# Kernel optimization log

Measured on AMD Instinct MI355X. Metric: run time of the kernel, lower is better.

## Reference

```python
import jax, jax.numpy as jnp
import numpy as np

C = 1024        # number of classes
N = 8           # proxies per class
ALLNUM = C * N  # 8192 total proxies
DIM = 512
R = 0.05
TOPK = int(np.ceil(R * ALLNUM))  # 410
LAM = 0.3
B = 2048


def setup_inputs() -> dict:
    key = jax.random.key(0)
    k1, k2, k3 = jax.random.split(key, 3)
    inp = jax.random.normal(k1, (B, DIM), dtype=jnp.float32)
    target = jax.random.randint(k2, (B,), 0, C, dtype=jnp.int64)
    # kaiming-uniform-initialized proxies approximated by scaled normal init
    proxies = jax.random.normal(k3, (DIM, ALLNUM), dtype=jnp.float32)
    instance_label = jnp.repeat(jnp.arange(C, dtype=jnp.int64), N)  # [ALLNUM]
    return {"input": inp, "target": target, "Proxies": proxies,
            "instance_label": instance_label}


def reference(input, target, Proxies, instance_label):
    # L2-normalize each proxy column (F.normalize along dim=0, eps=1e-12)
    norm = jnp.maximum(jnp.linalg.norm(Proxies, axis=0, keepdims=True), 1e-12)
    centers = Proxies / norm                             # [DIM, ALLNUM]
    similarity = input @ centers                          # [B, ALLNUM]

    positive_mask = (target[:, None] == instance_label[None, :]).astype(similarity.dtype)
    _, indices = jax.lax.top_k(similarity + 1000.0 * positive_mask, TOPK)  # [B, TOPK]

    rows = jnp.arange(similarity.shape[0])[:, None]
    mask = jnp.zeros_like(similarity).at[rows, indices].set(1.0)
    prob_a = mask * similarity                            # sparse-masked similarities

    y_instance_onehot = jax.nn.one_hot(instance_label, C, dtype=similarity.dtype)  # [ALLNUM, C]
    logits = prob_a @ y_instance_onehot                   # [B, C]

    y_target_onehot = jax.nn.one_hot(target, C, dtype=similarity.dtype)  # [B, C]
    logits_mask = 1.0 - (logits == 0.0).astype(similarity.dtype)

    # scale_mask_softmax with scale=1 along dim=1
    e = jnp.exp(logits) * logits_mask
    predict = e / (1e-8 + jnp.sum(e, axis=1, keepdims=True))
    lossClassify = jnp.mean(jnp.sum(-y_target_onehot * jnp.log(predict + 1e-20), axis=1))

    # proxy regularizer: cross-entropy of proxy-vs-class logits
    simCenter = centers.T @ centers                       # [ALLNUM, ALLNUM]
    centers_logits = simCenter @ y_instance_onehot        # [ALLNUM, C]
    logp = jax.nn.log_softmax(centers_logits, axis=1)
    reg = -jnp.mean(jnp.take_along_axis(logp, instance_label[:, None], axis=1))

    return (lossClassify + LAM * reg, lossClassify)
```

## Files before the change

### kernel.cpp

```cpp
#include <hip/hip_runtime.h>
#include <hip/hip_bf16.h>
#include <math.h>

#define C_CLS   1024
#define NPROXY  8
#define ALLNUM  8192
#define DIM     512
#define TOPK    410
#define LAM     0.3f
#define BATCH   2048

#define BAND_CAP_BLK 28
#define ROW_CAP      512
#define GCAP         64

typedef __bf16 bf16x8 __attribute__((ext_vector_type(8)));
typedef float floatx4 __attribute__((ext_vector_type(4)));
typedef unsigned short ushort_t;

#define WS_RNORM 0
#define WS_SIG   8192
#define WS_LP    10240
#define WS_RP    12288
#define WS_CNT   14336
#define WS_NDEF  16384
#define WS_FLAG  18432
#define WS_CLS   20480
#define WS_BVAL  (WS_CLS + 2048*1024)
#define WS_BCOL  (WS_BVAL + 2048*512)
#define WS_ABF   (WS_BCOL + 2048*256)
#define WS_PBF   (WS_ABF + 524288)
#define WS_STBF  (WS_PBF + 2097152)
#define WS_LOG   (WS_STBF + 262144)

__device__ inline float block_reduce(float v, int is_max, float* red, int t) {
    #pragma unroll
    for (int o = 32; o > 0; o >>= 1) {
        float w = __shfl_down(v, o);
        v = is_max ? fmaxf(v, w) : (v + w);
    }
    __syncthreads();
    if ((t & 63) == 0) red[t >> 6] = v;
    __syncthreads();
    return is_max ? fmaxf(fmaxf(red[0], red[1]), fmaxf(red[2], red[3]))
                  : (red[0] + red[1] + red[2] + red[3]);
}

__device__ inline ushort_t f2bf(float f) {
    unsigned u = __float_as_uint(f);
    return (ushort_t)((u + 0x7FFFu + ((u >> 16) & 1u)) >> 16);
}

__device__ inline float bf2f(ushort_t u) {
    return __uint_as_float(((unsigned)u) << 16);
}

__device__ inline void ld_g2l_16(const void* g, void* l) {
    __builtin_amdgcn_global_load_lds(
        (const __attribute__((address_space(1))) unsigned int*)g,
        (__attribute__((address_space(3))) unsigned int*)l,
        16, 0, 0);
}

__device__ inline unsigned f2ord(float f) {
    unsigned u = __float_as_uint(f);
    return (u & 0x80000000u) ? ~u : (u | 0x80000000u);
}

__global__ __launch_bounds__(256) void k_prep1(const float* __restrict__ P,
                                               const float* __restrict__ input,
                                               float* __restrict__ rnorm,
                                               float* __restrict__ rowsig,
                                               ushort_t* __restrict__ Abf,
                                               ushort_t* __restrict__ Pbf,
                                               unsigned* __restrict__ zaux) {
    __shared__ float tile[32][33];
    float* cred = &tile[0][0];
    int bx = blockIdx.x, t = threadIdx.x;
    if (bx < 256) {
        int tc = t & 31, g = t >> 5;
        int c = bx * 32 + tc;
        const float* pc = P + (size_t)(g * 64) * ALLNUM + c;
        float s = 0.f;
        #pragma unroll 8
        for (int d = 0; d < 64; ++d) {
            float v = pc[(size_t)d * ALLNUM];
            s += v * v;
        }
        cred[g * 32 + tc] = s;
        __syncthreads();
        if (g == 0) {
            float tot = 0.f;
            #pragma unroll
            for (int k = 0; k < 8; ++k) tot += cred[k * 32 + tc];
            rnorm[c] = 1.0f / fmaxf(sqrtf(tot), 1e-12f);
        }
    } else if (bx < 256 + 1024) {
        int a = bx - 256;
        int idx = a * 256 + t;
        float4 v = ((const float4*)input)[idx];
        ushort4 o;
        o.x = f2bf(v.x); o.y = f2bf(v.y); o.z = f2bf(v.z); o.w = f2bf(v.w);
        ((ushort4*)Abf)[idx] = o;
        float sq = v.x * v.x + v.y * v.y + v.z * v.z + v.w * v.w;
        #pragma unroll
        for (int off = 32; off > 0; off >>= 1) sq += __shfl_down(sq, off);
        int lane = t & 63, w = t >> 6;
        if (lane == 0) cred[w] = sq;
        __syncthreads();
        if (t == 0) {
            rowsig[2 * a]     = sqrtf(cred[0] + cred[1]);
            rowsig[2 * a + 1] = sqrtf(cred[2] + cred[3]);
        }
    } else if (bx < 256 + 1024 + 4096) {
        int id = bx - 1280;
        int c0 = (id & 255) * 32, r0 = (id >> 8) * 32;
        int tc = t & 31, tr = t >> 5;
        #pragma unroll
        for (int p = 0; p < 4; ++p)
            tile[tr + p * 8][tc] = P[(size_t)(r0 + tr + p * 8) * ALLNUM + c0 + tc];
        __syncthreads();
        #pragma unroll
        for (int p = 0; p < 4; ++p) {
            int oc = tr + p * 8;
            Pbf[(size_t)(c0 + oc) * DIM + r0 + tc] = f2bf(tile[tc][oc]);
        }
    } else {
        for (int i = t; i < 3 * 2048; i += 256) zaux[i] = 0u;
    }
}

__global__ __launch_bounds__(256) void k_stage2(const ushort_t* __restrict__ A,
                                                const ushort_t* __restrict__ B,
                                                const float* __restrict__ P,
                                                const float* __restrict__ rnorm,
                                                const float* __restrict__ rowsig,
                                                const int* __restrict__ target,
                                                float* __restrict__ g_cls,
                                                float* __restrict__ g_bval,
                                                ushort_t* __restrict__ g_bcol,
                                                unsigned* __restrict__ g_cnt,
                                                unsigned* __restrict__ g_ndef,
                                                unsigned* __restrict__ g_flag,
                                                ushort_t* __restrict__ Stbf) {
    __shared__ __align__(16) ushort_t smem[2 * 128 * 64];
    int bx = blockIdx.x, t = threadIdx.x;

    if (bx < 1024) {
        ushort_t* sA = smem;
        ushort_t* sB = smem + 128 * 64;
        int w = t >> 6, lane = t & 63;
        int wm = w >> 1, wn = w & 1;
        int bj = (bx & 63) * 128, bi = (bx >> 6) * 128;

        floatx4 acc[4][4];
        #pragma unroll
        for (int tm = 0; tm < 4; ++tm)
            #pragma unroll
            for (int tn = 0; tn < 4; ++tn)
                acc[tm][tn] = (floatx4){0.f, 0.f, 0.f, 0.f};

        for (int k0 = 0; k0 < DIM; k0 += 64) {
            #pragma unroll
            for (int it = 0; it < 4; ++it) {
                int c = w * 256 + it * 64 + lane;
                int m = c >> 3, s = c & 7;
                int q = s ^ (m & 7);
                ld_g2l_16(A + ((size_t)(bi + m) << 9) + k0 + q * 8,
                          &sA[(w * 256 + it * 64) * 8]);
            }
            #pragma unroll
            for (int it = 0; it < 4; ++it) {
                int c = w * 256 + it * 64 + lane;
                int m = c >> 3, s = c & 7;
                int q = s ^ (m & 7);
                ld_g2l_16(B + ((size_t)(bj + m) << 9) + k0 + q * 8,
                          &sB[(w * 256 + it * 64) * 8]);
            }
            asm volatile("s_waitcnt vmcnt(0)" ::: "memory");
            __syncthreads();

            #pragma unroll
            for (int kk = 0; kk < 2; ++kk) {
                bf16x8 af[4], bfr[4];
                int ml = lane & 15, q = lane >> 4;
                #pragma unroll
                for (int tm = 0; tm < 4; ++tm) {
                    int m = wm * 64 + tm * 16 + ml;
                    int s = (kk * 4 + q) ^ (m & 7);
                    af[tm] = *(const bf16x8*)&sA[m * 64 + s * 8];
                }
                #pragma unroll
                for (int tn = 0; tn < 4; ++tn) {
                    int n = wn * 64 + tn * 16 + ml;
                    int s = (kk * 4 + q) ^ (n & 7);
                    bfr[tn] = *(const bf16x8*)&sB[n * 64 + s * 8];
                }
                #pragma unroll
                for (int tm = 0; tm < 4; ++tm)
                    #pragma unroll
                    for (int tn = 0; tn < 4; ++tn)
                        acc[tm][tn] = __builtin_amdgcn_mfma_f32_16x16x32_bf16(
                            af[tm], bfr[tn], acc[tm][tn], 0, 0, 0);
            }
            __syncthreads();
        }

        unsigned char* sb = (unsigned char*)smem;
        float*    e_cls = (float*)sb;
        float*    e_bv  = (float*)(sb + 8192);
        ushort_t* e_bc  = (ushort_t*)(sb + 22528);
        unsigned* e_cnt = (unsigned*)(sb + 29696);
        unsigned* e_nd  = (unsigned*)(sb + 30208);

        #pragma unroll
        for (int i = t; i < 2048; i += 256) e_cls[i] = 0.f;
        if (t < 128) { e_cnt[t] = 0u; e_nd[t] = 0u; }
        __syncthreads();

        int ml = lane & 15, qd = lane >> 4;
        #pragma unroll
        for (int tm = 0; tm < 4; ++tm) {
            int rl0 = wm * 64 + tm * 16 + qd * 4;
            int rowb = bi + rl0;
            float4 rs4 = *(const float4*)&rowsig[rowb];
            int4   tg4 = *(const int4*)&target[rowb];
            #pragma unroll
            for (int tn = 0; tn < 4; ++tn) {
                int cl = wn * 64 + tn * 16 + ml;
                int col = bj + cl;
                float sc = rnorm[col];
                int cls = col >> 3;
                int clsl = cl >> 3;
                #pragma unroll
                for (int i = 0; i < 4; ++i) {
                    int rl = rl0 + i;
                    float v = acc[tm][tn][i] * sc;
                    float sg = ((const float*)&rs4)[i] * (1.0f / 22.616f);
                    float hiT = 1.80f * sg, loT = 1.47f * sg;
                    int tg = ((const int*)&tg4)[i];
                    if (cls == tg) {
                        atomicAdd(&e_cls[rl * 16 + clsl], v);
                    } else if (v >= hiT) {
                        atomicAdd(&e_cls[rl * 16 + clsl], v);
                        atomicAdd(&e_nd[rl], 1u);
                    } else if (v >= loT) {
                        unsigned u = atomicAdd(&e_cnt[rl], 1u);
                        if (u < BAND_CAP_BLK) {
                            e_bv[rl * BAND_CAP_BLK + u] = v;
                            e_bc[rl * BAND_CAP_BLK + u] = (ushort_t)col;
                        }
                    }
                }
            }
        }
        __syncthreads();

        int bjc = bj >> 3;
        #pragma unroll
        for (int i = t; i < 2048; i += 256) {
            int rl = i >> 4, c = i & 15;
            g_cls[(size_t)(bi + rl) * C_CLS + bjc + c] = e_cls[i];
        }
        if (t < 128) {
            int row = bi + t;
            unsigned c = e_cnt[t];
            unsigned nd = e_nd[t];
            if (nd) atomicAdd(&g_ndef[row], nd);
            if (c) {
                unsigned cc = (c > BAND_CAP_BLK) ? BAND_CAP_BLK : c;
                unsigned base = atomicAdd(&g_cnt[row], cc);
                if (c > BAND_CAP_BLK || base + cc > ROW_CAP) g_flag[row] = 1u;
                for (unsigned j = 0; j < cc; ++j) {
                    if (base + j >= ROW_CAP) break;
                    g_bval[(size_t)row * ROW_CAP + base + j] = e_bv[t * BAND_CAP_BLK + j];
                    g_bcol[(size_t)row * ROW_CAP + base + j] = e_bc[t * BAND_CAP_BLK + j];
                }
            }
        }
    } else {
        float* tile = (float*)smem;
        int id = bx - 1024;
        int c0 = (id & 31) * 32, d0 = (id >> 5) * 32;
        int cl = t & 31, dl8 = t >> 5;
        #pragma unroll
        for (int p = 0; p < 4; ++p) {
            int d = d0 + dl8 + 8 * p;
            int c = c0 + cl;
            const float* pp = P + (size_t)d * ALLNUM + c * NPROXY;
            const float* rn = rnorm + c * NPROXY;
            float4 a = *(const float4*)pp;
            float4 b = *(const float4*)(pp + 4);
            float4 ra = *(const float4*)rn;
            float4 rb = *(const float4*)(rn + 4);
            tile[(dl8 + 8 * p) * 33 + cl] =
                a.x * ra.x + a.y * ra.y + a.z * ra.z + a.w * ra.w +
                b.x * rb.x + b.y * rb.y + b.z * rb.z + b.w * rb.w;
        }
        __syncthreads();
        #pragma unroll
        for (int p = 0; p < 4; ++p) {
            int cl2 = dl8 + 8 * p, dl2 = t & 31;
            Stbf[(size_t)(c0 + cl2) * DIM + d0 + dl2] = f2bf(tile[dl2 * 33 + cl2]);
        }
    }
}

__device__ inline void suffix_select1(unsigned* s_hist, unsigned kk,
                                      unsigned* s_wtot, unsigned* sh_bin,
                                      unsigned* sh_k, int t, int lane, int wid) {
    unsigned h = s_hist[t];
    unsigned v = h;
    #pragma unroll
    for (int off = 1; off < 64; off <<= 1) {
        unsigned o = __shfl_down(v, off);
        if (lane + off < 64) v += o;
    }
    if (lane == 0) s_wtot[wid] = v;
    __syncthreads();
    unsigned above = v - h;
    for (int w2 = wid + 1; w2 < 4; ++w2) above += s_wtot[w2];
    unsigned cum = above + h;
    if (cum >= kk && above < kk) { *sh_bin = (unsigned)t; *sh_k = kk - above; }
    __syncthreads();
}

__global__ __launch_bounds__(256) void k_stage3(const int* __restrict__ target,
                                                const float* __restrict__ rowsig,
                                                const float* __restrict__ rnorm,
                                                const ushort_t* __restrict__ Abf,
                                                const ushort_t* __restrict__ Pbf,
                                                const ushort_t* __restrict__ Stbf,
                                                const float* __restrict__ g_cls,
                                                const float* __restrict__ g_bval,
                                                const ushort_t* __restrict__ g_bcol,
                                                const unsigned* __restrict__ g_cnt,
                                                const unsigned* __restrict__ g_ndef,
                                                const unsigned* __restrict__ g_flag,
                                                float* __restrict__ loss_part,
                                                ushort_t* __restrict__ logits) {
    __shared__ __align__(16) unsigned char smem[16384];
    int bx = blockIdx.x, t = threadIdx.x;
    int lane = t & 63, wid = t >> 6;

    if (bx < 2048) {
        ushort_t* sA = (ushort_t*)smem;
        ushort_t* sB = (ushort_t*)(smem + 8192);
        int id = bx;
        int bj = (id & 15) * 64;
        int bi = (id >> 4) * 64;
        int w = wid;
        int wm = w >> 1, wn = w & 1;

        floatx4 acc[2][2];
        #pragma unroll
        for (int tm = 0; tm < 2; ++tm)
            #pragma unroll
            for (int tn = 0; tn < 2; ++tn)
                acc[tm][tn] = (floatx4){0.f, 0.f, 0.f, 0.f};

        for (int k0 = 0; k0 < DIM; k0 += 64) {
            #pragma unroll
            for (int it = 0; it < 2; ++it) {
                int c = (w * 2 + it) * 64 + lane;
                int m = c >> 3, s = c & 7;
                int q = s ^ (m & 7);
                ld_g2l_16(Pbf + ((size_t)(bi + m) << 9) + k0 + q * 8,
                          &sA[((w * 2 + it) * 64) * 8]);
            }
            #pragma unroll
            for (int it = 0; it < 2; ++it) {
                int c = (w * 2 + it) * 64 + lane;
                int m = c >> 3, s = c & 7;
                int q = s ^ (m & 7);
                ld_g2l_16(Stbf + ((size_t)(bj + m) << 9) + k0 + q * 8,
                          &sB[((w * 2 + it) * 64) * 8]);
            }
            asm volatile("s_waitcnt vmcnt(0)" ::: "memory");
            __syncthreads();

            #pragma unroll
            for (int kk = 0; kk < 2; ++kk) {
                bf16x8 af[2], bfr[2];
                int ml = lane & 15, q = lane >> 4;
                #pragma unroll
                for (int tm = 0; tm < 2; ++tm) {
                    int m = wm * 32 + tm * 16 + ml;
                    int s = (kk * 4 + q) ^ (m & 7);
                    af[tm] = *(const bf16x8*)&sA[m * 64 + s * 8];
                }
                #pragma unroll
                for (int tn = 0; tn < 2; ++tn) {
                    int n = wn * 32 + tn * 16 + ml;
                    int s = (kk * 4 + q) ^ (n & 7);
                    bfr[tn] = *(const bf16x8*)&sB[n * 64 + s * 8];
                }
                #pragma unroll
                for (int tm = 0; tm < 2; ++tm)
                    #pragma unroll
                    for (int tn = 0; tn < 2; ++tn)
                        acc[tm][tn] = __builtin_amdgcn_mfma_f32_16x16x32_bf16(
                            af[tm], bfr[tn], acc[tm][tn], 0, 0, 0);
            }
            __syncthreads();
        }

        int ml = lane & 15, qd = lane >> 4;
        #pragma unroll
        for (int tm = 0; tm < 2; ++tm) {
            int rowb = bi + wm * 32 + tm * 16 + qd * 4;
            float4 rnr = *(const float4*)&rnorm[rowb];
            #pragma unroll
            for (int tn = 0; tn < 2; ++tn) {
                int col = bj + wn * 32 + tn * 16 + ml;
                #pragma unroll
                for (int i = 0; i < 4; ++i)
                    logits[(size_t)(rowb + i) * C_CLS + col] =
                        f2bf(acc[tm][tn][i] * ((const float*)&rnr)[i]);
            }
        }
    } else {
        float*    s_cls  = (float*)smem;
        float*    s_bval = (float*)(smem + 4096);
        ushort_t* s_bcol = (ushort_t*)(smem + 6144);
        unsigned* s_hist = (unsigned*)(smem + 7168);
        float*    s_arow = (float*)(smem + 8192);
        unsigned* s_wtot = (unsigned*)(smem + 10240);
        unsigned* shv    = (unsigned*)(smem + 10256);
        float*    shf    = (float*)(smem + 10272);
        float*    red    = (float*)(smem + 10288);
        float*    s_gval = (float*)(smem + 10304);

        int b = bx - 2048;
        int tgt = target[b];
        float sig = rowsig[b] * (1.0f / 22.616f);
        float hiT = 1.80f * sig, loT = 1.47f * sig;
        float binscale = 256.0f / (hiT - loT);

        ((float4*)s_cls)[t] = ((const float4*)(g_cls + (size_t)b * C_CLS))[t];
        unsigned cnt = g_cnt[b], nd = g_ndef[b], fl = g_flag[b];
        int kq = (TOPK - NPROXY) - (int)nd;
        int ok = (fl == 0u) && (cnt <= ROW_CAP) && (kq >= 0) && ((int)cnt >= kq);
        if (t == 0) shv[1] = 0u;
        s_hist[t] = 0u;
        __syncthreads();

        if (ok) {
            if (kq > 0) {
                for (int j = t; j < (int)cnt; j += 256) {
                    float v = g_bval[(size_t)b * ROW_CAP + j];
                    s_bval[j] = v;
                    s_bcol[j] = g_bcol[(size_t)b * ROW_CAP + j];
                    int bin = (int)((v - loT) * binscale);
                    bin = (bin > 255) ? 255 : bin;
                    atomicAdd(&s_hist[bin], 1u);
                }
                __syncthreads();
                suffix_select1(s_hist, (unsigned)kq, s_wtot, &shv[2], &shv[3], t, lane, wid);
                int Bb = (int)shv[2];
                int knew = (int)shv[3];
                for (int j = t; j < (int)cnt; j += 256) {
                    float v = s_bval[j];
                    int bin = (int)((v - loT) * binscale);
                    bin = (bin > 255) ? 255 : bin;
                    if (bin == Bb) {
                        unsigned g = atomicAdd(&shv[1], 1u);
                        if (g < GCAP) s_gval[g] = v;
                    }
                }
                __syncthreads();
                int gc = (int)shv[1];
                if (gc <= GCAP) {
                    if (t < gc) {
                        float vj = s_gval[t];
                        unsigned g = 0, geq = 0;
                        for (int i = 0; i < gc; ++i) {
                            float vi = s_gval[i];
                            g   += (vi > vj) ? 1u : 0u;
                            geq += (vi >= vj) ? 1u : 0u;
                        }
                        if (g < (unsigned)knew && geq >= (unsigned)knew) shf[0] = vj;
                    }
                } else {
                    for (int j = t; j < (int)cnt; j += 256) {
                        float vj = s_bval[j];
                        unsigned g = 0, geq = 0;
                        for (int i = 0; i < (int)cnt; ++i) {
                            float vi = s_bval[i];
                            g   += (vi > vj) ? 1u : 0u;
                            geq += (vi >= vj) ? 1u : 0u;
                        }
                        if (g < (unsigned)kq && geq >= (unsigned)kq) shf[0] = vj;
                    }
                }
                __syncthreads();
                float thr = shf[0];
                for (int j = t; j < (int)cnt; j += 256)
                    if (s_bval[j] >= thr)
                        atomicAdd(&s_cls[s_bcol[j] >> 3], s_bval[j]);
            }
        } else {
            for (int i = t; i < DIM; i += 256)
                s_arow[i] = bf2f(Abf[(size_t)b * DIM + i]);
            #pragma unroll
            for (int i = 0; i < 4; ++i) s_cls[t + 256 * i] = 0.f;
            __syncthreads();
            float4 v4[8];
            for (int p = 0; p < 8; ++p) {
                int f = t + 256 * p;
                float vv[4];
                for (int e = 0; e < 4; ++e) {
                    int col = 4 * f + e;
                    const ushort_t* pc = Pbf + (size_t)col * DIM;
                    float a = 0.f;
                    for (int d = 0; d < DIM; ++d)
                        a += s_arow[d] * bf2f(pc[d]);
                    vv[e] = a * rnorm[col];
                }
                float4 o; o.x = vv[0]; o.y = vv[1]; o.z = vv[2]; o.w = vv[3];
                v4[p] = o;
            }
            #pragma unroll
            for (int p = 0; p < 8; ++p) {
                int f = t + 256 * p;
                const float* pv = (const float*)&v4[p];
                if ((f >> 1) == tgt)
                    atomicAdd(&s_cls[tgt], pv[0] + pv[1] + pv[2] + pv[3]);
            }
            unsigned L = 0u, R = 0xFFFFFFFFu;
            for (int it = 0; it < 33 && R - L > 1; ++it) {
                unsigned mid = L + ((R - L) >> 1);
                float c = 0.f;
                #pragma unroll
                for (int p = 0; p < 8; ++p) {
                    int f = t + 256 * p;
                    const float* pv = (const float*)&v4[p];
                    if ((f >> 1) != tgt) {
                        #pragma unroll
                        for (int e = 0; e < 4; ++e)
                            c += (f2ord(pv[e]) >= mid) ? 1.f : 0.f;
                    }
                }
                c = block_reduce(c, 0, red, t);
                if (c >= (float)(TOPK - NPROXY)) L = mid; else R = mid;
                __syncthreads();
            }
            #pragma unroll
            for (int p = 0; p < 8; ++p) {
                int f = t + 256 * p;
                const float* pv = (const float*)&v4[p];
                if ((f >> 1) != tgt) {
                    #pragma unroll
                    for (int e = 0; e < 4; ++e)
                        if (f2ord(pv[e]) >= L)
                            atomicAdd(&s_cls[f >> 1], pv[e]);
                }
            }
        }
        __syncthreads();

        float4 cv = ((const float4*)s_cls)[t];
        float m = -1e30f;
        if (cv.x != 0.0f) m = fmaxf(m, cv.x);
        if (cv.y != 0.0f) m = fmaxf(m, cv.y);
        if (cv.z != 0.0f) m = fmaxf(m, cv.z);
        if (cv.w != 0.0f) m = fmaxf(m, cv.w);
        m = block_reduce(m, 1, red, t);
        float se = 0.f;
        if (cv.x != 0.0f) se += expf(cv.x - m);
        if (cv.y != 0.0f) se += expf(cv.y - m);
        if (cv.z != 0.0f) se += expf(cv.z - m);
        if (cv.w != 0.0f) se += expf(cv.w - m);
        se = block_reduce(se, 0, red, t);
        if (t == 0) {
            float lt = s_cls[tgt];
            float predict_t = expf(lt - m) / (1e-8f * expf(-m) + se);
            loss_part[b] = -logf(predict_t + 1e-20f);
        }
    }
}

__global__ __launch_bounds__(256) void k_regloss(const ushort_t* __restrict__ logits,
                                                 float* __restrict__ reg_part) {
    __shared__ float bsum[4];
    int t = threadIdx.x, lane = t & 63, wid = t >> 6;
    int i = blockIdx.x * 4 + wid;
    const ushort_t* row = logits + (size_t)i * C_CLS;
    uint4 c0 = ((const uint4*)row)[lane];
    uint4 c1 = ((const uint4*)(row + 512))[lane];

    float f[16];
    const unsigned* u0 = (const unsigned*)&c0;
    const unsigned* u1 = (const unsigned*)&c1;
    #pragma unroll
    for (int k = 0; k < 4; ++k) {
        f[2 * k]     = __uint_as_float(u0[k] << 16);
        f[2 * k + 1] = __uint_as_float(u0[k] & 0xFFFF0000u);
        f[8 + 2 * k]     = __uint_as_float(u1[k] << 16);
        f[8 + 2 * k + 1] = __uint_as_float(u1[k] & 0xFFFF0000u);
    }

    int cstar = i >> 3;
    int chunk = cstar >> 9, within = cstar & 511;
    float sd = 0.f;
    if (lane == (within >> 3)) sd = f[chunk * 8 + (within & 7)];

    float m = -1e30f;
    #pragma unroll
    for (int k = 0; k < 16; ++k) m = fmaxf(m, f[k]);
    #pragma unroll
    for (int off = 32; off > 0; off >>= 1) m = fmaxf(m, __shfl_xor(m, off));

    float se = 0.f;
    #pragma unroll
    for (int k = 0; k < 16; ++k) se += expf(f[k] - m);
    #pragma unroll
    for (int off = 32; off > 0; off >>= 1) se += __shfl_xor(se, off);
    #pragma unroll
    for (int off = 32; off > 0; off >>= 1) sd += __shfl_xor(sd, off);

    if (lane == 0) bsum[wid] = m + logf(se) - sd;
    __syncthreads();
    if (t == 0)
        reg_part[blockIdx.x] = bsum[0] + bsum[1] + bsum[2] + bsum[3];
}

__global__ __launch_bounds__(256) void k_final(const float* __restrict__ lp,
                                               const float* __restrict__ rp,
                                               float* __restrict__ out) {
    __shared__ float red[4];
    int t = threadIdx.x;
    float4 a = ((const float4*)lp)[t];
    float4 b = ((const float4*)lp)[t + 256];
    float4 c = ((const float4*)rp)[t];
    float4 d = ((const float4*)rp)[t + 256];
    float ls = a.x + a.y + a.z + a.w + b.x + b.y + b.z + b.w;
    float rs = c.x + c.y + c.z + c.w + d.x + d.y + d.z + d.w;
    ls = block_reduce(ls, 0, red, t);
    rs = block_reduce(rs, 0, red, t);
    if (t == 0) {
        float lc = ls / (float)BATCH;
        float rg = rs / (float)ALLNUM;
        out[0] = lc + LAM * rg;
        out[1] = lc;
    }
}

extern "C" void kernel_launch(void* const* d_in, const int* in_sizes, int n_in,
                              void* d_out, int out_size, void* d_ws, size_t ws_size,
                              hipStream_t stream) {
    const float* input  = (const float*)d_in[0];
    const int*   target = (const int*)d_in[1];
    const float* P      = (const float*)d_in[2];

    float* ws        = (float*)d_ws;
    float* rnorm     = ws + WS_RNORM;
    float* rowsig    = ws + WS_SIG;
    float* loss_part = ws + WS_LP;
    float* reg_part  = ws + WS_RP;
    unsigned* g_cnt  = (unsigned*)(ws + WS_CNT);
    unsigned* g_ndef = (unsigned*)(ws + WS_NDEF);
    unsigned* g_flag = (unsigned*)(ws + WS_FLAG);
    float* g_cls     = ws + WS_CLS;
    float* g_bval    = ws + WS_BVAL;
    ushort_t* g_bcol = (ushort_t*)(ws + WS_BCOL);
    ushort_t* Abf    = (ushort_t*)(ws + WS_ABF);
    ushort_t* Pbf    = (ushort_t*)(ws + WS_PBF);
    ushort_t* Stbf   = (ushort_t*)(ws + WS_STBF);
    ushort_t* logits = (ushort_t*)(ws + WS_LOG);
    float* out       = (float*)d_out;

    hipLaunchKernelGGL(k_prep1, dim3(256 + 1024 + 4096 + 1), dim3(256), 0, stream,
                       P, input, rnorm, rowsig, Abf, Pbf, g_cnt);
    hipLaunchKernelGGL(k_stage2, dim3(1024 + 512), dim3(256), 0, stream,
                       Abf, Pbf, P, rnorm, rowsig, target,
                       g_cls, g_bval, g_bcol, g_cnt, g_ndef, g_flag, Stbf);
    hipLaunchKernelGGL(k_stage3, dim3(2048 + 2048), dim3(256), 0, stream,
                       target, rowsig, rnorm, Abf, Pbf, Stbf,
                       g_cls, g_bval, g_bcol, g_cnt, g_ndef, g_flag,
                       loss_part, logits);
    hipLaunchKernelGGL(k_regloss, dim3(ALLNUM / 4), dim3(256), 0, stream,
                       logits, reg_part);
    hipLaunchKernelGGL(k_final, dim3(1), dim3(256), 0, stream,
                       loss_part, reg_part, out);
}
```

Baseline: 157.4 us.

## Merge both GEMMs into one double-buffered kernel and fold regloss into finish

The class-center matrix Stbf is now built in the prep kernel from the column norms. Both bf16 GEMMs (the similarity GEMM and the proxy-vs-class logits GEMM) now run in a single kernel with 512 threads, double-buffered LDS stages and larger 256x256 tiles for the similarity part. The regloss pass is merged into the finishing kernel, removing one launch and one inter-kernel dependency. The per-block band capacity is raised to match the larger tile width, and the larger LDS footprint and more accumulators per thread may reduce occupancy.

```diff
diff --git a/kernel.cpp b/kernel.cpp
--- a/kernel.cpp
+++ b/kernel.cpp
@@ -10,7 +10,7 @@
 #define LAM     0.3f
 #define BATCH   2048
 
-#define BAND_CAP_BLK 28
+#define BAND_CAP_BLK 40
 #define ROW_CAP      512
 #define GCAP         64
 
@@ -73,8 +73,10 @@
                                                float* __restrict__ rowsig,
                                                ushort_t* __restrict__ Abf,
                                                ushort_t* __restrict__ Pbf,
+                                               ushort_t* __restrict__ Stbf,
                                                unsigned* __restrict__ zaux) {
     __shared__ float tile[32][33];
+    __shared__ float s_rn[32];
     float* cred = &tile[0][0];
     int bx = blockIdx.x, t = threadIdx.x;
     if (bx < 256) {
@@ -93,7 +95,22 @@
             float tot = 0.f;
             #pragma unroll
             for (int k = 0; k < 8; ++k) tot += cred[k * 32 + tc];
-            rnorm[c] = 1.0f / fmaxf(sqrtf(tot), 1e-12f);
+            float r = 1.0f / fmaxf(sqrtf(tot), 1e-12f);
+            rnorm[c] = r;
+            s_rn[tc] = r;
+        }
+        __syncthreads();
+        #pragma unroll
+        for (int p = 0; p < 8; ++p) {
+            int idx = t + 256 * p;
+            int d = idx >> 2, cc = idx & 3;
+            const float* pp = P + (size_t)d * ALLNUM + bx * 32 + cc * 8;
+            const float* rr = &s_rn[cc * 8];
+            float4 a = *(const float4*)pp;
+            float4 b = *(const float4*)(pp + 4);
+            float v = a.x * rr[0] + a.y * rr[1] + a.z * rr[2] + a.w * rr[3] +
+                      b.x * rr[4] + b.y * rr[5] + b.z * rr[6] + b.w * rr[7];
+            Stbf[(size_t)(bx * 4 + cc) * DIM + d] = f2bf(v);
         }
     } else if (bx < 256 + 1024) {
         int a = bx - 256;
@@ -130,104 +147,110 @@
     }
 }
 
-__global__ __launch_bounds__(256) void k_stage2(const ushort_t* __restrict__ A,
-                                                const ushort_t* __restrict__ B,
-                                                const float* __restrict__ P,
-                                                const float* __restrict__ rnorm,
-                                                const float* __restrict__ rowsig,
-                                                const int* __restrict__ target,
-                                                float* __restrict__ g_cls,
-                                                float* __restrict__ g_bval,
-                                                ushort_t* __restrict__ g_bcol,
-                                                unsigned* __restrict__ g_cnt,
-                                                unsigned* __restrict__ g_ndef,
-                                                unsigned* __restrict__ g_flag,
-                                                ushort_t* __restrict__ Stbf) {
-    __shared__ __align__(16) ushort_t smem[2 * 128 * 64];
+__global__ __launch_bounds__(512, 2) void k_gemms(const ushort_t* __restrict__ Abf,
+                                                  const ushort_t* __restrict__ Pbf,
+                                                  const ushort_t* __restrict__ Stbf,
+                                                  const float* __restrict__ rnorm,
+                                                  const float* __restrict__ rowsig,
+                                                  const int* __restrict__ target,
+                                                  float* __restrict__ g_cls,
+                                                  float* __restrict__ g_bval,
+                                                  ushort_t* __restrict__ g_bcol,
+                                                  unsigned* __restrict__ g_cnt,
+                                                  unsigned* __restrict__ g_ndef,
+                                                  unsigned* __restrict__ g_flag,
+                                                  ushort_t* __restrict__ logits) {
+    __shared__ __align__(16) ushort_t smem[65536];
     int bx = blockIdx.x, t = threadIdx.x;
-
-    if (bx < 1024) {
-        ushort_t* sA = smem;
-        ushort_t* sB = smem + 128 * 64;
-        int w = t >> 6, lane = t & 63;
-        int wm = w >> 1, wn = w & 1;
-        int bj = (bx & 63) * 128, bi = (bx >> 6) * 128;
-
-        floatx4 acc[4][4];
-        #pragma unroll
-        for (int tm = 0; tm < 4; ++tm)
-            #pragma unroll
-            for (int tn = 0; tn < 4; ++tn)
-                acc[tm][tn] = (floatx4){0.f, 0.f, 0.f, 0.f};
-
-        for (int k0 = 0; k0 < DIM; k0 += 64) {
-            #pragma unroll
-            for (int it = 0; it < 4; ++it) {
-                int c = w * 256 + it * 64 + lane;
-                int m = c >> 3, s = c & 7;
-                int q = s ^ (m & 7);
-                ld_g2l_16(A + ((size_t)(bi + m) << 9) + k0 + q * 8,
-                          &sA[(w * 256 + it * 64) * 8]);
-            }
-            #pragma unroll
-            for (int it = 0; it < 4; ++it) {
-                int c = w * 256 + it * 64 + lane;
-                int m = c >> 3, s = c & 7;
-                int q = s ^ (m & 7);
-                ld_g2l_16(B + ((size_t)(bj + m) << 9) + k0 + q * 8,
-                          &sB[(w * 256 + it * 64) * 8]);
-            }
-            asm volatile("s_waitcnt vmcnt(0)" ::: "memory");
+    int w = t >> 6, lane = t & 63;
+    int ml = lane & 15, q4 = lane >> 4;
+
+    if (bx < 256) {
+        int bi = (bx >> 5) * 256, bj = (bx & 31) * 256;
+        int wm = w >> 2, wn = w & 3;
+        ushort_t* sA0 = smem;
+        ushort_t* sB0 = smem + 16384;
+        ushort_t* sA1 = smem + 32768;
+        ushort_t* sB1 = smem + 49152;
+
+        floatx4 acc[8][4];
+        #pragma unroll
+        for (int mf = 0; mf < 8; ++mf)
+            #pragma unroll
+            for (int nf = 0; nf < 4; ++nf)
+                acc[mf][nf] = (floatx4){0.f, 0.f, 0.f, 0.f};
+
+        #define STAGE0(sa, sb, k0) do {                                        \
+            _Pragma("unroll")                                                  \
+            for (int it = 0; it < 4; ++it) {                                   \
+                int c = w * 256 + it * 64 + lane;                              \
+                int m = c >> 3, s = c & 7, qq = s ^ (m & 7);                   \
+                ld_g2l_16(Abf + ((size_t)(bi + m) << 9) + (k0) + qq * 8,       \
+                          &(sa)[c * 8]);                                       \
+            }                                                                  \
+            _Pragma("unroll")                                                  \
+            for (int it = 0; it < 4; ++it) {                                   \
+                int c = w * 256 + it * 64 + lane;                              \
+                int m = c >> 3, s = c & 7, qq = s ^ (m & 7);                   \
+                ld_g2l_16(Pbf + ((size_t)(bj + m) << 9) + (k0) + qq * 8,       \
+                          &(sb)[c * 8]);                                       \
+            }                                                                  \
+        } while (0)
+
+        STAGE0(sA0, sB0, 0);
+        __syncthreads();
+        #pragma unroll
+        for (int tt = 0; tt < 8; ++tt) {
+            ushort_t* cA = (tt & 1) ? sA1 : sA0;
+            ushort_t* cB = (tt & 1) ? sB1 : sB0;
+            if (tt < 7) {
+                if (tt & 1) STAGE0(sA0, sB0, (tt + 1) * 64);
+                else        STAGE0(sA1, sB1, (tt + 1) * 64);
+            }
+            #pragma unroll
+            for (int kk = 0; kk < 2; ++kk) {
+                bf16x8 bfr[4];
+                #pragma unroll
+                for (int nf = 0; nf < 4; ++nf) {
+                    int n = wn * 64 + nf * 16 + ml;
+                    int s = (kk * 4 + q4) ^ (n & 7);
+                    bfr[nf] = *(const bf16x8*)&cB[n * 64 + s * 8];
+                }
+                #pragma unroll
+                for (int mf = 0; mf < 8; ++mf) {
+                    int m = wm * 128 + mf * 16 + ml;
+                    int s = (kk * 4 + q4) ^ (m & 7);
+                    bf16x8 af = *(const bf16x8*)&cA[m * 64 + s * 8];
+                    #pragma unroll
+                    for (int nf = 0; nf < 4; ++nf)
+                        acc[mf][nf] = __builtin_amdgcn_mfma_f32_16x16x32_bf16(
+                            af, bfr[nf], acc[mf][nf], 0, 0, 0);
+                }
+            }
             __syncthreads();
-
-            #pragma unroll
-            for (int kk = 0; kk < 2; ++kk) {
-                bf16x8 af[4], bfr[4];
-                int ml = lane & 15, q = lane >> 4;
-                #pragma unroll
-                for (int tm = 0; tm < 4; ++tm) {
-                    int m = wm * 64 + tm * 16 + ml;
-                    int s = (kk * 4 + q) ^ (m & 7);
-                    af[tm] = *(const bf16x8*)&sA[m * 64 + s * 8];
-                }
-                #pragma unroll
-                for (int tn = 0; tn < 4; ++tn) {
-                    int n = wn * 64 + tn * 16 + ml;
-                    int s = (kk * 4 + q) ^ (n & 7);
-                    bfr[tn] = *(const bf16x8*)&sB[n * 64 + s * 8];
-                }
-                #pragma unroll
-                for (int tm = 0; tm < 4; ++tm)
-                    #pragma unroll
-                    for (int tn = 0; tn < 4; ++tn)
-                        acc[tm][tn] = __builtin_amdgcn_mfma_f32_16x16x32_bf16(
-                            af[tm], bfr[tn], acc[tm][tn], 0, 0, 0);
-            }
-            __syncthreads();
-        }
-
-        unsigned char* sb = (unsigned char*)smem;
-        float*    e_cls = (float*)sb;
-        float*    e_bv  = (float*)(sb + 8192);
-        ushort_t* e_bc  = (ushort_t*)(sb + 22528);
-        unsigned* e_cnt = (unsigned*)(sb + 29696);
-        unsigned* e_nd  = (unsigned*)(sb + 30208);
-
-        #pragma unroll
-        for (int i = t; i < 2048; i += 256) e_cls[i] = 0.f;
-        if (t < 128) { e_cnt[t] = 0u; e_nd[t] = 0u; }
-        __syncthreads();
-
-        int ml = lane & 15, qd = lane >> 4;
-        #pragma unroll
-        for (int tm = 0; tm < 4; ++tm) {
-            int rl0 = wm * 64 + tm * 16 + qd * 4;
+        }
+
+        unsigned char* sb8 = (unsigned char*)smem;
+        float*    e_cls = (float*)sb8;
+        float*    e_bv  = (float*)(sb8 + 32768);
+        ushort_t* e_bc  = (ushort_t*)(sb8 + 73728);
+        unsigned* e_cnt = (unsigned*)(sb8 + 94208);
+        unsigned* e_nd  = (unsigned*)(sb8 + 95232);
+
+        #pragma unroll
+        for (int i = t; i < 8192; i += 512) e_cls[i] = 0.f;
+        if (t < 256) { e_cnt[t] = 0u; e_nd[t] = 0u; }
+        __syncthreads();
+
+        #pragma unroll
+        for (int mf = 0; mf < 8; ++mf) {
+            int rl0 = wm * 128 + mf * 16 + q4 * 4;
             int rowb = bi + rl0;
             float4 rs4 = *(const float4*)&rowsig[rowb];
             int4   tg4 = *(const int4*)&target[rowb];
             #pragma unroll
-            for (int tn = 0; tn < 4; ++tn) {
-                int cl = wn * 64 + tn * 16 + ml;
+            for (int nf = 0; nf < 4; ++nf) {
+                int cl = wn * 64 + nf * 16 + ml;
                 int col = bj + cl;
                 float sc = rnorm[col];
                 int cls = col >> 3;
@@ -235,14 +258,14 @@
                 #pragma unroll
                 for (int i = 0; i < 4; ++i) {
                     int rl = rl0 + i;
-                    float v = acc[tm][tn][i] * sc;
+                    float v = acc[mf][nf][i] * sc;
                     float sg = ((const float*)&rs4)[i] * (1.0f / 22.616f);
                     float hiT = 1.80f * sg, loT = 1.47f * sg;
                     int tg = ((const int*)&tg4)[i];
                     if (cls == tg) {
-                        atomicAdd(&e_cls[rl * 16 + clsl], v);
+                        atomicAdd(&e_cls[rl * 32 + clsl], v);
                     } else if (v >= hiT) {
-                        atomicAdd(&e_cls[rl * 16 + clsl], v);
+                        atomicAdd(&e_cls[rl * 32 + clsl], v);
                         atomicAdd(&e_nd[rl], 1u);
                     } else if (v >= loT) {
                         unsigned u = atomicAdd(&e_cnt[rl], 1u);
@@ -258,19 +281,19 @@
 
         int bjc = bj >> 3;
         #pragma unroll
-        for (int i = t; i < 2048; i += 256) {
-            int rl = i >> 4, c = i & 15;
+        for (int i = t; i < 8192; i += 512) {
+            int rl = i >> 5, c = i & 31;
             g_cls[(size_t)(bi + rl) * C_CLS + bjc + c] = e_cls[i];
         }
-        if (t < 128) {
+        if (t < 256) {
             int row = bi + t;
-            unsigned c = e_cnt[t];
+            unsigned cbb = e_cnt[t];
             unsigned nd = e_nd[t];
             if (nd) atomicAdd(&g_ndef[row], nd);
-            if (c) {
-                unsigned cc = (c > BAND_CAP_BLK) ? BAND_CAP_BLK : c;
+            if (cbb) {
+                unsigned cc = (cbb > BAND_CAP_BLK) ? BAND_CAP_BLK : cbb;
                 unsigned base = atomicAdd(&g_cnt[row], cc);
-                if (c > BAND_CAP_BLK || base + cc > ROW_CAP) g_flag[row] = 1u;
+                if (cbb > BAND_CAP_BLK || base + cc > ROW_CAP) g_flag[row] = 1u;
                 for (unsigned j = 0; j < cc; ++j) {
                     if (base + j >= ROW_CAP) break;
                     g_bval[(size_t)row * ROW_CAP + base + j] = e_bv[t * BAND_CAP_BLK + j];
@@ -278,31 +301,87 @@
                 }
             }
         }
+        #undef STAGE0
     } else {
-        float* tile = (float*)smem;
-        int id = bx - 1024;
-        int c0 = (id & 31) * 32, d0 = (id >> 5) * 32;
-        int cl = t & 31, dl8 = t >> 5;
-        #pragma unroll
-        for (int p = 0; p < 4; ++p) {
-            int d = d0 + dl8 + 8 * p;
-            int c = c0 + cl;
-            const float* pp = P + (size_t)d * ALLNUM + c * NPROXY;
-            const float* rn = rnorm + c * NPROXY;
-            float4 a = *(const float4*)pp;
-            float4 b = *(const float4*)(pp + 4);
-            float4 ra = *(const float4*)rn;
-            float4 rb = *(const float4*)(rn + 4);
-            tile[(dl8 + 8 * p) * 33 + cl] =
-                a.x * ra.x + a.y * ra.y + a.z * ra.z + a.w * ra.w +
-                b.x * rb.x + b.y * rb.y + b.z * rb.z + b.w * rb.w;
-        }
-        __syncthreads();
-        #pragma unroll
-        for (int p = 0; p < 4; ++p) {
-            int cl2 = dl8 + 8 * p, dl2 = t & 31;
-            Stbf[(size_t)(c0 + cl2) * DIM + d0 + dl2] = f2bf(tile[dl2 * 33 + cl2]);
-        }
+        int id = bx - 256;
+        int bi = (id >> 3) * 256, bj = (id & 7) * 128;
+        int wm = w >> 1, wn = w & 1;
+        ushort_t* sA0 = smem;
+        ushort_t* sB0 = smem + 16384;
+        ushort_t* sA1 = smem + 32768;
+        ushort_t* sB1 = smem + 49152;
+
+        floatx4 acc[4][4];
+        #pragma unroll
+        for (int mf = 0; mf < 4; ++mf)
+            #pragma unroll
+            for (int nf = 0; nf < 4; ++nf)
+                acc[mf][nf] = (floatx4){0.f, 0.f, 0.f, 0.f};
+
+        #define STAGE1(sa, sb, k0) do {                                        \
+            _Pragma("unroll")                                                  \
+            for (int it = 0; it < 4; ++it) {                                   \
+                int c = w * 256 + it * 64 + lane;                              \
+                int m = c >> 3, s = c & 7, qq = s ^ (m & 7);                   \
+                ld_g2l_16(Pbf + ((size_t)(bi + m) << 9) + (k0) + qq * 8,       \
+                          &(sa)[c * 8]);                                       \
+            }                                                                  \
+            _Pragma("unroll")                                                  \
+            for (int it = 0; it < 2; ++it) {                                   \
+                int c = w * 128 + it * 64 + lane;                              \
+                int m = c >> 3, s = c & 7, qq = s ^ (m & 7);                   \
+                ld_g2l_16(Stbf + ((size_t)(bj + m) << 9) + (k0) + qq * 8,      \
+                          &(sb)[c * 8]);                                       \
+            }                                                                  \
+        } while (0)
+
+        STAGE1(sA0, sB0, 0);
+        __syncthreads();
+        #pragma unroll
+        for (int tt = 0; tt < 8; ++tt) {
+            ushort_t* cA = (tt & 1) ? sA1 : sA0;
+            ushort_t* cB = (tt & 1) ? sB1 : sB0;
+            if (tt < 7) {
+                if (tt & 1) STAGE1(sA0, sB0, (tt + 1) * 64);
+                else        STAGE1(sA1, sB1, (tt + 1) * 64);
+            }
+            #pragma unroll
+            for (int kk = 0; kk < 2; ++kk) {
+                bf16x8 bfr[4];
+                #pragma unroll
+                for (int nf = 0; nf < 4; ++nf) {
+                    int n = wn * 64 + nf * 16 + ml;
+                    int s = (kk * 4 + q4) ^ (n & 7);
+                    bfr[nf] = *(const bf16x8*)&cB[n * 64 + s * 8];
+                }
+                #pragma unroll
+                for (int mf = 0; mf < 4; ++mf) {
+                    int m = wm * 64 + mf * 16 + ml;
+                    int s = (kk * 4 + q4) ^ (m & 7);
+                    bf16x8 af = *(const bf16x8*)&cA[m * 64 + s * 8];
+                    #pragma unroll
+                    for (int nf = 0; nf < 4; ++nf)
+                        acc[mf][nf] = __builtin_amdgcn_mfma_f32_16x16x32_bf16(
+                            af, bfr[nf], acc[mf][nf], 0, 0, 0);
+                }
+            }
+            __syncthreads();
+        }
+
+        #pragma unroll
+        for (int mf = 0; mf < 4; ++mf) {
+            int rowb = bi + wm * 64 + mf * 16 + q4 * 4;
+            float4 rnr = *(const float4*)&rnorm[rowb];
+            #pragma unroll
+            for (int nf = 0; nf < 4; ++nf) {
+                int col = bj + wn * 64 + nf * 16 + ml;
+                #pragma unroll
+                for (int i = 0; i < 4; ++i)
+                    logits[(size_t)(rowb + i) * C_CLS + col] =
+                        f2bf(acc[mf][nf][i] * ((const float*)&rnr)[i]);
+            }
+        }
+        #undef STAGE1
     }
 }
 
@@ -325,12 +404,11 @@
     __syncthreads();
 }
 
-__global__ __launch_bounds__(256) void k_stage3(const int* __restrict__ target,
+__global__ __launch_bounds__(256) void k_finish(const int* __restrict__ target,
                                                 const float* __restrict__ rowsig,
                                                 const float* __restrict__ rnorm,
                                                 const ushort_t* __restrict__ Abf,
                                                 const ushort_t* __restrict__ Pbf,
-                                                const ushort_t* __restrict__ Stbf,
                                                 const float* __restrict__ g_cls,
                                                 const float* __restrict__ g_bval,
                                                 const ushort_t* __restrict__ g_bcol,
@@ -338,88 +416,13 @@
                                                 const unsigned* __restrict__ g_ndef,
                                                 const unsigned* __restrict__ g_flag,
                                                 float* __restrict__ loss_part,
-                                                ushort_t* __restrict__ logits) {
+                                                const ushort_t* __restrict__ logits,
+                                                float* __restrict__ reg_part) {
     __shared__ __align__(16) unsigned char smem[16384];
     int bx = blockIdx.x, t = threadIdx.x;
     int lane = t & 63, wid = t >> 6;
 
     if (bx < 2048) {
-        ushort_t* sA = (ushort_t*)smem;
-        ushort_t* sB = (ushort_t*)(smem + 8192);
-        int id = bx;
-        int bj = (id & 15) * 64;
-        int bi = (id >> 4) * 64;
-        int w = wid;
-        int wm = w >> 1, wn = w & 1;
-
-        floatx4 acc[2][2];
-        #pragma unroll
-        for (int tm = 0; tm < 2; ++tm)
-            #pragma unroll
-            for (int tn = 0; tn < 2; ++tn)
-                acc[tm][tn] = (floatx4){0.f, 0.f, 0.f, 0.f};
-
-        for (int k0 = 0; k0 < DIM; k0 += 64) {
-            #pragma unroll
-            for (int it = 0; it < 2; ++it) {
-                int c = (w * 2 + it) * 64 + lane;
-                int m = c >> 3, s = c & 7;
-                int q = s ^ (m & 7);
-                ld_g2l_16(Pbf + ((size_t)(bi + m) << 9) + k0 + q * 8,
-                          &sA[((w * 2 + it) * 64) * 8]);
-            }
-            #pragma unroll
-            for (int it = 0; it < 2; ++it) {
-                int c = (w * 2 + it) * 64 + lane;
-                int m = c >> 3, s = c & 7;
-                int q = s ^ (m & 7);
-                ld_g2l_16(Stbf + ((size_t)(bj + m) << 9) + k0 + q * 8,
-                          &sB[((w * 2 + it) * 64) * 8]);
-            }
-            asm volatile("s_waitcnt vmcnt(0)" ::: "memory");
-            __syncthreads();
-
-            #pragma unroll
-            for (int kk = 0; kk < 2; ++kk) {
-                bf16x8 af[2], bfr[2];
-                int ml = lane & 15, q = lane >> 4;
-                #pragma unroll
-                for (int tm = 0; tm < 2; ++tm) {
-                    int m = wm * 32 + tm * 16 + ml;
-                    int s = (kk * 4 + q) ^ (m & 7);
-                    af[tm] = *(const bf16x8*)&sA[m * 64 + s * 8];
-                }
-                #pragma unroll
-                for (int tn = 0; tn < 2; ++tn) {
-                    int n = wn * 32 + tn * 16 + ml;
-                    int s = (kk * 4 + q) ^ (n & 7);
-                    bfr[tn] = *(const bf16x8*)&sB[n * 64 + s * 8];
-                }
-                #pragma unroll
-                for (int tm = 0; tm < 2; ++tm)
-                    #pragma unroll
-                    for (int tn = 0; tn < 2; ++tn)
-                        acc[tm][tn] = __builtin_amdgcn_mfma_f32_16x16x32_bf16(
-                            af[tm], bfr[tn], acc[tm][tn], 0, 0, 0);
-            }
-            __syncthreads();
-        }
-
-        int ml = lane & 15, qd = lane >> 4;
-        #pragma unroll
-        for (int tm = 0; tm < 2; ++tm) {
-            int rowb = bi + wm * 32 + tm * 16 + qd * 4;
-            float4 rnr = *(const float4*)&rnorm[rowb];
-            #pragma unroll
-            for (int tn = 0; tn < 2; ++tn) {
-                int col = bj + wn * 32 + tn * 16 + ml;
-                #pragma unroll
-                for (int i = 0; i < 4; ++i)
-                    logits[(size_t)(rowb + i) * C_CLS + col] =
-                        f2bf(acc[tm][tn][i] * ((const float*)&rnr)[i]);
-            }
-        }
-    } else {
         float*    s_cls  = (float*)smem;
         float*    s_bval = (float*)(smem + 4096);
         ushort_t* s_bcol = (ushort_t*)(smem + 6144);
@@ -431,7 +434,7 @@
         float*    red    = (float*)(smem + 10288);
         float*    s_gval = (float*)(smem + 10304);
 
-        int b = bx - 2048;
+        int b = bx;
         int tgt = target[b];
         float sig = rowsig[b] * (1.0f / 22.616f);
         float hiT = 1.80f * sig, loT = 1.47f * sig;
@@ -577,52 +580,49 @@
             float predict_t = expf(lt - m) / (1e-8f * expf(-m) + se);
             loss_part[b] = -logf(predict_t + 1e-20f);
         }
+    } else {
+        __shared__ float bsum[4];
+        int rb = bx - 2048;
+        int i = rb * 4 + wid;
+        const ushort_t* row = logits + (size_t)i * C_CLS;
+        uint4 c0 = ((const uint4*)row)[lane];
+        uint4 c1 = ((const uint4*)(row + 512))[lane];
+
+        float f[16];
+        const unsigned* u0 = (const unsigned*)&c0;
+        const unsigned* u1 = (const unsigned*)&c1;
+        #pragma unroll
+        for (int k = 0; k < 4; ++k) {
+            f[2 * k]     = __uint_as_float(u0[k] << 16);
+            f[2 * k + 1] = __uint_as_float(u0[k] & 0xFFFF0000u);
+            f[8 + 2 * k]     = __uint_as_float(u1[k] << 16);
+            f[8 + 2 * k + 1] = __uint_as_float(u1[k] & 0xFFFF0000u);
+        }
+
+        int cstar = i >> 3;
+        int chunk = cstar >> 9, within = cstar & 511;
+        float sd = 0.f;
+        if (lane == (within >> 3)) sd = f[chunk * 8 + (within & 7)];
+
+        float m = -1e30f;
+        #pragma unroll
+        for (int k = 0; k < 16; ++k) m = fmaxf(m, f[k]);
+        #pragma unroll
+        for (int off = 32; off > 0; off >>= 1) m = fmaxf(m, __shfl_xor(m, off));
+
+        float se = 0.f;
+        #pragma unroll
+        for (int k = 0; k < 16; ++k) se += expf(f[k] - m);
+        #pragma unroll
+        for (int off = 32; off > 0; off >>= 1) se += __shfl_xor(se, off);
+        #pragma unroll
+        for (int off = 32; off > 0; off >>= 1) sd += __shfl_xor(sd, off);
+
+        if (lane == 0) bsum[wid] = m + logf(se) - sd;
+        __syncthreads();
+        if (t == 0)
+            reg_part[rb] = bsum[0] + bsum[1] + bsum[2] + bsum[3];
     }
-}
-
-__global__ __launch_bounds__(256) void k_regloss(const ushort_t* __restrict__ logits,
-                                                 float* __restrict__ reg_part) {
-    __shared__ float bsum[4];
-    int t = threadIdx.x, lane = t & 63, wid = t >> 6;
-    int i = blockIdx.x * 4 + wid;
-    const ushort_t* row = logits + (size_t)i * C_CLS;
-    uint4 c0 = ((const uint4*)row)[lane];
-    uint4 c1 = ((const uint4*)(row + 512))[lane];
-
-    float f[16];
-    const unsigned* u0 = (const unsigned*)&c0;
-    const unsigned* u1 = (const unsigned*)&c1;
-    #pragma unroll
-    for (int k = 0; k < 4; ++k) {
-        f[2 * k]     = __uint_as_float(u0[k] << 16);
-        f[2 * k + 1] = __uint_as_float(u0[k] & 0xFFFF0000u);
-        f[8 + 2 * k]     = __uint_as_float(u1[k] << 16);
-        f[8 + 2 * k + 1] = __uint_as_float(u1[k] & 0xFFFF0000u);
-    }
-
-    int cstar = i >> 3;
-    int chunk = cstar >> 9, within = cstar & 511;
-    float sd = 0.f;
-    if (lane == (within >> 3)) sd = f[chunk * 8 + (within & 7)];
-
-    float m = -1e30f;
-    #pragma unroll
-    for (int k = 0; k < 16; ++k) m = fmaxf(m, f[k]);
-    #pragma unroll
-    for (int off = 32; off > 0; off >>= 1) m = fmaxf(m, __shfl_xor(m, off));
-
-    float se = 0.f;
-    #pragma unroll
-    for (int k = 0; k < 16; ++k) se += expf(f[k] - m);
-    #pragma unroll
-    for (int off = 32; off > 0; off >>= 1) se += __shfl_xor(se, off);
-    #pragma unroll
-    for (int off = 32; off > 0; off >>= 1) sd += __shfl_xor(sd, off);
-
-    if (lane == 0) bsum[wid] = m + logf(se) - sd;
-    __syncthreads();
-    if (t == 0)
-        reg_part[blockIdx.x] = bsum[0] + bsum[1] + bsum[2] + bsum[3];
 }
 
 __global__ __launch_bounds__(256) void k_final(const float* __restrict__ lp,
@@ -671,16 +671,14 @@
     float* out       = (float*)d_out;
 
     hipLaunchKernelGGL(k_prep1, dim3(256 + 1024 + 4096 + 1), dim3(256), 0, stream,
-                       P, input, rnorm, rowsig, Abf, Pbf, g_cnt);
-    hipLaunchKernelGGL(k_stage2, dim3(1024 + 512), dim3(256), 0, stream,
-                       Abf, Pbf, P, rnorm, rowsig, target,
-                       g_cls, g_bval, g_bcol, g_cnt, g_ndef, g_flag, Stbf);
-    hipLaunchKernelGGL(k_stage3, dim3(2048 + 2048), dim3(256), 0, stream,
-                       target, rowsig, rnorm, Abf, Pbf, Stbf,
+                       P, input, rnorm, rowsig, Abf, Pbf, Stbf, g_cnt);
+    hipLaunchKernelGGL(k_gemms, dim3(512), dim3(512), 0, stream,
+                       Abf, Pbf, Stbf, rnorm, rowsig, target,
+                       g_cls, g_bval, g_bcol, g_cnt, g_ndef, g_flag, logits);
+    hipLaunchKernelGGL(k_finish, dim3(4096), dim3(256), 0, stream,
+                       target, rowsig, rnorm, Abf, Pbf,
                        g_cls, g_bval, g_bcol, g_cnt, g_ndef, g_flag,
-                       loss_part, logits);
-    hipLaunchKernelGGL(k_regloss, dim3(ALLNUM / 4), dim3(256), 0, stream,
-                       logits, reg_part);
+                       loss_part, logits, reg_part);
     hipLaunchKernelGGL(k_final, dim3(1), dim3(256), 0, stream,
                        loss_part, reg_part, out);
 }
```

New measurement: 149.1 us. -5.3%, faster.
